# Optimization experiments

Measured on AMD Instinct MI355X. Metric: run time of the kernel, lower is better.

## Reference

```python
import jax, jax.numpy as jnp
import numpy as np
from jax import lax

T = 262144
H = 64
OUT = 16  # 2**MEMORY_LENGTH with MEMORY_LENGTH=4


def setup_inputs() -> dict:
    key = jax.random.key(0)
    ks = jax.random.split(key, 11)
    s = 0.1  # keep gates out of saturation
    return {
        "y": jax.random.normal(ks[0], (T, 1), jnp.float32),
        "W_ih0": s * jax.random.normal(ks[1], (4 * H, 1), jnp.float32),
        "W_hh0": s * jax.random.normal(ks[2], (4 * H, H), jnp.float32),
        "b_ih0": s * jax.random.normal(ks[3], (4 * H,), jnp.float32),
        "b_hh0": s * jax.random.normal(ks[4], (4 * H,), jnp.float32),
        "W_ih1": s * jax.random.normal(ks[5], (4 * H, H), jnp.float32),
        "W_hh1": s * jax.random.normal(ks[6], (4 * H, H), jnp.float32),
        "b_ih1": s * jax.random.normal(ks[7], (4 * H,), jnp.float32),
        "b_hh1": s * jax.random.normal(ks[8], (4 * H,), jnp.float32),
        "W_lin": s * jax.random.normal(ks[9], (OUT, H), jnp.float32),
        "b_lin": s * jax.random.normal(ks[10], (OUT,), jnp.float32),
    }


def _lstm_layer(x, W_ih, W_hh, b_ih, b_hh):
    # x: [T, in]. PyTorch gate order: i, f, g, o. Zero initial state.
    h = W_hh.shape[1]
    xp = x @ W_ih.T + (b_ih + b_hh)  # precompute input contribution: [T, 4H]

    def step(carry, xt):
        h_t, c_t = carry
        gates = xt + h_t @ W_hh.T
        i, f, g, o = jnp.split(gates, 4)
        i = jax.nn.sigmoid(i)
        f = jax.nn.sigmoid(f)
        g = jnp.tanh(g)
        o = jax.nn.sigmoid(o)
        c_new = f * c_t + i * g
        h_new = o * jnp.tanh(c_new)
        return (h_new, c_new), h_new

    init = (jnp.zeros((h,), x.dtype), jnp.zeros((h,), x.dtype))
    _, hs = lax.scan(step, init, xp)
    return hs  # [T, H]


def reference(y, W_ih0, W_hh0, b_ih0, b_hh0, W_ih1, W_hh1, b_ih1, b_hh1, W_lin, b_lin):
    # phase == 'train' branch of RNNDetector.forward
    h1 = _lstm_layer(y, W_ih0, W_hh0, b_ih0, b_hh0)   # [T, 64]
    h2 = _lstm_layer(h1, W_ih1, W_hh1, b_ih1, b_hh1)  # [T, 64]
    return h2 @ W_lin.T + b_lin                        # [T, 16]
```

## Files before the change

kernel.cpp:

```cpp
#include <hip/hip_runtime.h>


constexpr int T  = 262144;
constexpr int B  = 32;
constexpr int NB = T / B;
constexpr int RS = 2 * B;
constexpr int K_SS = NB + 3;

typedef _Float16 h2v  __attribute__((ext_vector_type(2)));
typedef _Float16 f16x8 __attribute__((ext_vector_type(8)));
typedef unsigned u4   __attribute__((ext_vector_type(4)));
typedef float    f4   __attribute__((ext_vector_type(4)));

__device__ __forceinline__ float rcp_f(float x) { return __builtin_amdgcn_rcpf(x); }

#define BARRIER() asm volatile("s_waitcnt lgkmcnt(0)\n\ts_barrier" ::: "memory")

static __device__ __forceinline__ float fd(unsigned w, unsigned h, float acc) {
#if __has_builtin(__builtin_amdgcn_fdot2)
  return __builtin_amdgcn_fdot2(__builtin_bit_cast(h2v, w),
                                __builtin_bit_cast(h2v, h), acc, false);
#else
  h2v a = __builtin_bit_cast(h2v, w), b = __builtin_bit_cast(h2v, h);
  acc = fmaf((float)a.x, (float)b.x, acc);
  acc = fmaf((float)a.y, (float)b.y, acc);
  return acc;
#endif
}
#define DP4(acc, W, H) { acc = fd((W).x, (H).x, acc); acc = fd((W).y, (H).y, acc); \
                         acc = fd((W).z, (H).z, acc); acc = fd((W).w, (H).w, acc); }

__device__ __forceinline__ f4 mf(u4 a, u4 b, f4 c) {
  return __builtin_amdgcn_mfma_f32_16x16x32_f16(
      __builtin_bit_cast(f16x8, a), __builtin_bit_cast(f16x8, b), c, 0, 0, 0);
}

__device__ __forceinline__ float sel4(float x0, float x1, float x2, float x3,
                                      bool b0, bool b1) {
  float lo = b0 ? x1 : x0;
  float hi = b0 ? x3 : x2;
  return b1 ? hi : lo;
}

#define DPPX1(x) __builtin_bit_cast(float, __builtin_amdgcn_mov_dpp(            \
                    __builtin_bit_cast(int, (x)), 0xB1, 0xF, 0xF, true))
#define DPPX2(x) __builtin_bit_cast(float, __builtin_amdgcn_mov_dpp(            \
                    __builtin_bit_cast(int, (x)), 0x4E, 0xF, 0xF, true))

__device__ __forceinline__ float exp2_f(float x) {
  float r; asm("v_exp_f32 %0, %1" : "=v"(r) : "v"(x)); return r;
}
__device__ __forceinline__ float exp2n_g(float u) {
  return exp2_f(fminf(-u, 126.f));
}
__device__ __forceinline__ float sig_u(float u)  { return rcp_f(1.f + exp2n_g(u)); }
__device__ __forceinline__ float tanh_u(float u) {
  float e2 = exp2n_g(u);
  return (1.f - e2) * rcp_f(1.f + e2);
}
__device__ __forceinline__ float tanh_c(float c) {
  return tanh_u(c * 2.8853900817779268f);
}

constexpr float L2E  = 1.4426950408889634f;
constexpr float L2E2 = 2.8853900817779268f;

__device__ unsigned f16rne(float f) {
  unsigned u = __float_as_uint(f);
  unsigned s = (u >> 16) & 0x8000u;
  int e = (int)((u >> 23) & 0xff) - 127;
  unsigned m = u & 0x7fffffu;
  if (e < -14) return s;
  unsigned h = s | (unsigned)((e + 15) << 10) | (m >> 13);
  unsigned rem = m & 0x1fffu;
  h += (rem > 0x1000u) || (rem == 0x1000u && (h & 1u));
  return h;
}

__global__ void pack_w(const float* __restrict__ Whh0,
                       const float* __restrict__ Whh1,
                       const float* __restrict__ Wih1,
                       const float* __restrict__ Wlin,
                       unsigned* __restrict__ ws) {
  int i = blockIdx.x * 256 + threadIdx.x;
  if (i >= 25088) return;
  float v0, v1, sc = 1.f;
  if (i < 24576) {
    int w = i >> 13, rem = i & 8191, l = rem >> 7, d = rem & 127;
    int n = d >> 3, s = (d >> 2) & 1, q = d & 3;
    int c = l & 15, g = l >> 4;
    int row = n * 16 + c;
    int col = s * 32 + 8 * g + 2 * q;
    const float* src = (w == 0) ? Whh0 : (w == 1) ? Whh1 : Wih1;
    v0 = src[row * 64 + col]; v1 = src[row * 64 + col + 1];
    sc = ((n >> 2) == 2) ? L2E2 : L2E;
  } else {
    int j = i - 24576, l = j >> 3, d = j & 7;
    int m = l >> 2, kq = l & 3, k = kq * 16 + 2 * d;
    v0 = Wlin[m * 64 + k]; v1 = Wlin[m * 64 + k + 1];
  }
  ws[i] = f16rne(v0 * sc) | (f16rne(v1 * sc) << 16);
}

#define DECLW32(wp)                                                            \
  u4 W0=(wp)[0],  W1=(wp)[1],  W2=(wp)[2],  W3=(wp)[3],                        \
     W4=(wp)[4],  W5=(wp)[5],  W6=(wp)[6],  W7=(wp)[7],                        \
     W8=(wp)[8],  W9=(wp)[9],  W10=(wp)[10],W11=(wp)[11],                      \
     W12=(wp)[12],W13=(wp)[13],W14=(wp)[14],W15=(wp)[15],                      \
     W16=(wp)[16],W17=(wp)[17],W18=(wp)[18],W19=(wp)[19],                      \
     W20=(wp)[20],W21=(wp)[21],W22=(wp)[22],W23=(wp)[23],                      \
     W24=(wp)[24],W25=(wp)[25],W26=(wp)[26],W27=(wp)[27],                      \
     W28=(wp)[28],W29=(wp)[29],W30=(wp)[30],W31=(wp)[31]

#define PINW8(a,b,c,d,e,f,g,h)                                                 \
  asm volatile("" : "+v"(a), "+v"(b), "+v"(c), "+v"(d),                        \
                    "+v"(e), "+v"(f), "+v"(g), "+v"(h))
#define PINALL() { PINW8(W0,W1,W2,W3,W4,W5,W6,W7);                             \
                   PINW8(W8,W9,W10,W11,W12,W13,W14,W15);                       \
                   PINW8(W16,W17,W18,W19,W20,W21,W22,W23);                     \
                   PINW8(W24,W25,W26,W27,W28,W29,W30,W31); }

#define MFMA16(A0u, A1u)                                                       \
  f4 a0  = mf(A0u, W0,  Z4); a0  = mf(A1u, W1,  a0);                           \
  f4 a1  = mf(A0u, W2,  Z4); a1  = mf(A1u, W3,  a1);                           \
  f4 a2  = mf(A0u, W4,  Z4); a2  = mf(A1u, W5,  a2);                           \
  f4 a3  = mf(A0u, W6,  Z4); a3  = mf(A1u, W7,  a3);                           \
  f4 a4  = mf(A0u, W8,  Z4); a4  = mf(A1u, W9,  a4);                           \
  f4 a5  = mf(A0u, W10, Z4); a5  = mf(A1u, W11, a5);                           \
  f4 a6  = mf(A0u, W12, Z4); a6  = mf(A1u, W13, a6);                           \
  f4 a7  = mf(A0u, W14, Z4); a7  = mf(A1u, W15, a7);                           \
  f4 a8  = mf(A0u, W16, Z4); a8  = mf(A1u, W17, a8);                           \
  f4 a9  = mf(A0u, W18, Z4); a9  = mf(A1u, W19, a9);                           \
  f4 a10 = mf(A0u, W20, Z4); a10 = mf(A1u, W21, a10);                          \
  f4 a11 = mf(A0u, W22, Z4); a11 = mf(A1u, W23, a11);                          \
  f4 a12 = mf(A0u, W24, Z4); a12 = mf(A1u, W25, a12);                          \
  f4 a13 = mf(A0u, W26, Z4); a13 = mf(A1u, W27, a13);                          \
  f4 a14 = mf(A0u, W28, Z4); a14 = mf(A1u, W29, a14);                          \
  f4 a15 = mf(A0u, W30, Z4); a15 = mf(A1u, W31, a15);

__global__ __launch_bounds__(256)
__attribute__((amdgpu_waves_per_eu(1, 1)))
void rnn_fused(
    const float* __restrict__ y,
    const float* __restrict__ Wih0, const float* __restrict__ bih0,
    const float* __restrict__ bhh0,
    const float* __restrict__ bih1, const float* __restrict__ bhh1,
    const float* __restrict__ blin,
    const unsigned* __restrict__ ws,
    float* __restrict__ out)
{
  const int tid = threadIdx.x;
  const int w = tid >> 6;
  __shared__ __align__(16) unsigned h0r[RS * 32];
  __shared__ __align__(16) unsigned h1r[RS * 32];
  __shared__ __align__(16) float    xpf[RS * 320];

  for (int j = tid; j < RS * 32; j += 256) { h0r[j] = 0u; h1r[j] = 0u; }
  __syncthreads();

  const f4 Z4 = {0.f, 0.f, 0.f, 0.f};

  if (w == 0) {
    __builtin_amdgcn_s_setprio(1);
    const int e = tid, g = e >> 4;
    const bool b0 = (g & 1) != 0, b1 = (g & 2) != 0;
    const u4* wp = (const u4*)(ws + e * 128);
    DECLW32(wp);
    float bbi = (bih0[e] + bhh0[e]) * L2E;
    float bbf = (bih0[64 + e] + bhh0[64 + e]) * L2E;
    float bbg = (bih0[128 + e] + bhh0[128 + e]) * L2E2;
    float bbo = (bih0[192 + e] + bhh0[192 + e]) * L2E;
    float wii = Wih0[e] * L2E, wif = Wih0[64 + e] * L2E;
    float wig = Wih0[128 + e] * L2E2, wio = Wih0[192 + e] * L2E;
    float c0 = 0.f;
    float ylv = y[e & (B - 1)];
    _Float16* h0h = (_Float16*)h0r;

    for (int k = 0; k < K_SS; ++k) {
      if (k < NB) {
        float yln = (k + 1 < NB) ? y[(k + 1) * B + (e & (B - 1))] : 0.f;
        const int base = k * B;
        #pragma unroll 1
        for (int i = 0; i < B; ++i) {
          const int s = base + i;
          PINALL();
          float ys = __builtin_bit_cast(float,
              __builtin_amdgcn_readlane(__builtin_bit_cast(int, ylv), i));
          const u4* ap = (const u4*)(h0r + ((s - 1) & (RS - 1)) * 32);
          u4 A0u = ap[g], A1u = ap[4 + g];
          MFMA16(A0u, A1u)
          float ti = sel4(a0[0],  a1[0],  a2[0],  a3[0],  b0, b1);
          float tf = sel4(a4[0],  a5[0],  a6[0],  a7[0],  b0, b1);
          float tg = sel4(a8[0],  a9[0],  a10[0], a11[0], b0, b1);
          float to = sel4(a12[0], a13[0], a14[0], a15[0], b0, b1);
          float I = sig_u(ti + fmaf(ys, wii, bbi));
          float F = sig_u(tf + fmaf(ys, wif, bbf));
          float G = tanh_u(tg + fmaf(ys, wig, bbg));
          float O = sig_u(to + fmaf(ys, wio, bbo));
          c0 = fmaf(F, c0, I * G);
          float h = O * tanh_c(c0);
          h0h[(s & (RS - 1)) * 64 + e] = (_Float16)h;
        }
        ylv = yln;
      }
      BARRIER();
    }
  } else if (w == 1 || w == 3) {
    const int e = tid & 63, g = e >> 4, c = e & 15;
    const bool b0 = (g & 1) != 0, b1 = (g & 2) != 0;
    const int ilo = (w == 1) ? 0 : 16;
    const u4* wp = (const u4*)(ws + 16384 + e * 128);
    DECLW32(wp);
    const u4* hwp = (const u4*)(ws + 24576 + e * 8);
    u4 HW0 = hwp[0], HW1 = hwp[1];
    float bbx, bby, bbz, bbw;
    {
      int R0 = (4 * g + 0) * 16 + c, R1 = (4 * g + 1) * 16 + c;
      int R2 = (4 * g + 2) * 16 + c, R3 = (4 * g + 3) * 16 + c;
      float s0 = (((4 * g + 0) >> 2) == 2) ? L2E2 : L2E;
      float s1 = (((4 * g + 1) >> 2) == 2) ? L2E2 : L2E;
      float s2 = (((4 * g + 2) >> 2) == 2) ? L2E2 : L2E;
      float s3 = (((4 * g + 3) >> 2) == 2) ? L2E2 : L2E;
      bbx = (bih1[R0] + bhh1[R0]) * s0; bby = (bih1[R1] + bhh1[R1]) * s1;
      bbz = (bih1[R2] + bhh1[R2]) * s2; bbw = (bih1[R3] + bhh1[R3]) * s3;
    }
    const int m = e >> 2, kq = e & 3;
    float bl = (kq == 0) ? blin[m] : 0.f;

    for (int k = 0; k < K_SS; ++k) {
      if (k >= 1 && k <= NB) {
        const int base = (k - 1) * B;
        #pragma unroll 1
        for (int i = ilo; i < ilo + 16; ++i) {
          const int t = base + i;
          const int slot = t & (RS - 1);
          PINALL();
          const u4* ap = (const u4*)(h0r + slot * 32);
          u4 A0u = ap[g], A1u = ap[4 + g];
          MFMA16(A0u, A1u)
          float vx = sel4(a0[0], a4[0], a8[0],  a12[0], b0, b1) + bbx;
          float vy = sel4(a1[0], a5[0], a9[0],  a13[0], b0, b1) + bby;
          float vz = sel4(a2[0], a6[0], a10[0], a14[0], b0, b1) + bbz;
          float vw = sel4(a3[0], a7[0], a11[0], a15[0], b0, b1) + bbw;
          f4 v = {vx, vy, vz, vw};
          *(f4*)(xpf + slot * 320 + c * 20 + 4 * g) = v;
        }
      }
      if (w == 3 && k >= 3) {
        const int base = (k - 3) * B;
        #pragma unroll 1
        for (int i = 0; i < B; ++i) {
          const int t = base + i;
          const int slot = t & (RS - 1);
          const u4* h1p = (const u4*)(h1r + slot * 32 + kq * 8);
          u4 X0 = h1p[0], X1 = h1p[1];
          float r2 = 0.f;
          DP4(r2, HW0, X0) DP4(r2, HW1, X1)
          r2 += DPPX1(r2);
          r2 += DPPX2(r2);
          if (kq == 0) out[t * 16 + m] = r2 + bl;
        }
      }
      BARRIER();
    }
  } else {
    __builtin_amdgcn_s_setprio(1);
    const int e = tid - 128, g = e >> 4, c = e & 15;
    const bool b0 = (g & 1) != 0, b1 = (g & 2) != 0;
    const u4* wp = (const u4*)(ws + 8192 + e * 128);
    DECLW32(wp);
    float c1 = 0.f;
    _Float16* h1h = (_Float16*)h1r;

    for (int k = 0; k < K_SS; ++k) {
      if (k >= 2 && k <= NB + 1) {
        const int base = (k - 2) * B;
        #pragma unroll 1
        for (int i = 0; i < B; ++i) {
          const int t = base + i;
          const int slot = t & (RS - 1);
          PINALL();
          const float* xb = xpf + slot * 320 + c * 20;
          float xi = xb[g], xf = xb[4 + g], xg2 = xb[8 + g], xo = xb[12 + g];
          const u4* ap = (const u4*)(h1r + ((t - 1) & (RS - 1)) * 32);
          u4 A0u = ap[g], A1u = ap[4 + g];
          MFMA16(A0u, A1u)
          float ti = sel4(a0[0],  a1[0],  a2[0],  a3[0],  b0, b1);
          float tf = sel4(a4[0],  a5[0],  a6[0],  a7[0],  b0, b1);
          float tg = sel4(a8[0],  a9[0],  a10[0], a11[0], b0, b1);
          float to = sel4(a12[0], a13[0], a14[0], a15[0], b0, b1);
          float I = sig_u(ti + xi);
          float F = sig_u(tf + xf);
          float G = tanh_u(tg + xg2);
          float O = sig_u(to + xo);
          c1 = fmaf(F, c1, I * G);
          float h = O * tanh_c(c1);
          h1h[slot * 64 + e] = (_Float16)h;
        }
      }
      BARRIER();
    }
  }
}

extern "C" void kernel_launch(void* const* d_in, const int* in_sizes, int n_in,
                              void* d_out, int out_size, void* d_ws, size_t ws_size,
                              hipStream_t stream) {
  const float* y    = (const float*)d_in[0];
  const float* Wih0 = (const float*)d_in[1];
  const float* Whh0 = (const float*)d_in[2];
  const float* bih0 = (const float*)d_in[3];
  const float* bhh0 = (const float*)d_in[4];
  const float* Wih1 = (const float*)d_in[5];
  const float* Whh1 = (const float*)d_in[6];
  const float* bih1 = (const float*)d_in[7];
  const float* bhh1 = (const float*)d_in[8];
  const float* Wlin = (const float*)d_in[9];
  const float* blin = (const float*)d_in[10];
  unsigned* ws = (unsigned*)d_ws;

  pack_w<<<dim3(98), dim3(256), 0, stream>>>(Whh0, Whh1, Wih1, Wlin, ws);
  rnn_fused<<<dim3(1), dim3(256), 0, stream>>>(
      y, Wih0, bih0, bhh0, bih1, bhh1, blin, ws, (float*)d_out);
}
```

Baseline: 109.2 ms.

## Fuse layer-0 and layer-1 recurrences into one wave with interleaved steps

New measurement: 208.4 ms. 90.9% more time.

```diff
diff --git a/kernel.cpp b/kernel.cpp
--- a/kernel.cpp
+++ b/kernel.cpp
@@ -11,6 +11,9 @@
 typedef _Float16 f16x8 __attribute__((ext_vector_type(8)));
 typedef unsigned u4   __attribute__((ext_vector_type(4)));
 typedef float    f4   __attribute__((ext_vector_type(4)));
+
+struct TT { static constexpr bool value = true; };
+struct FF { static constexpr bool value = false; };
 
 __device__ __forceinline__ float rcp_f(float x) { return __builtin_amdgcn_rcpf(x); }
 
@@ -112,13 +115,30 @@
      W24=(wp)[24],W25=(wp)[25],W26=(wp)[26],W27=(wp)[27],                      \
      W28=(wp)[28],W29=(wp)[29],W30=(wp)[30],W31=(wp)[31]
 
+#define DECLX32(wp)                                                            \
+  u4 X0=(wp)[0],  X1=(wp)[1],  X2=(wp)[2],  X3=(wp)[3],                        \
+     X4=(wp)[4],  X5=(wp)[5],  X6=(wp)[6],  X7=(wp)[7],                        \
+     X8=(wp)[8],  X9=(wp)[9],  X10=(wp)[10],X11=(wp)[11],                      \
+     X12=(wp)[12],X13=(wp)[13],X14=(wp)[14],X15=(wp)[15],                      \
+     X16=(wp)[16],X17=(wp)[17],X18=(wp)[18],X19=(wp)[19],                      \
+     X20=(wp)[20],X21=(wp)[21],X22=(wp)[22],X23=(wp)[23],                      \
+     X24=(wp)[24],X25=(wp)[25],X26=(wp)[26],X27=(wp)[27],                      \
+     X28=(wp)[28],X29=(wp)[29],X30=(wp)[30],X31=(wp)[31]
+
 #define PINW8(a,b,c,d,e,f,g,h)                                                 \
   asm volatile("" : "+v"(a), "+v"(b), "+v"(c), "+v"(d),                        \
                     "+v"(e), "+v"(f), "+v"(g), "+v"(h))
-#define PINALL() { PINW8(W0,W1,W2,W3,W4,W5,W6,W7);                             \
-                   PINW8(W8,W9,W10,W11,W12,W13,W14,W15);                       \
-                   PINW8(W16,W17,W18,W19,W20,W21,W22,W23);                     \
-                   PINW8(W24,W25,W26,W27,W28,W29,W30,W31); }
+#define PINA8(a,b,c,d,e,f,g,h)                                                 \
+  asm volatile("" : "+a"(a), "+a"(b), "+a"(c), "+a"(d),                        \
+                    "+a"(e), "+a"(f), "+a"(g), "+a"(h))
+#define PINALLW() { PINW8(W0,W1,W2,W3,W4,W5,W6,W7);                            \
+                    PINW8(W8,W9,W10,W11,W12,W13,W14,W15);                      \
+                    PINW8(W16,W17,W18,W19,W20,W21,W22,W23);                    \
+                    PINW8(W24,W25,W26,W27,W28,W29,W30,W31); }
+#define PINALLX() { PINA8(X0,X1,X2,X3,X4,X5,X6,X7);                            \
+                    PINA8(X8,X9,X10,X11,X12,X13,X14,X15);                      \
+                    PINA8(X16,X17,X18,X19,X20,X21,X22,X23);                    \
+                    PINA8(X24,X25,X26,X27,X28,X29,X30,X31); }
 
 #define MFMA16(A0u, A1u)                                                       \
   f4 a0  = mf(A0u, W0,  Z4); a0  = mf(A1u, W1,  a0);                           \
@@ -138,6 +158,24 @@
   f4 a14 = mf(A0u, W28, Z4); a14 = mf(A1u, W29, a14);                          \
   f4 a15 = mf(A0u, W30, Z4); a15 = mf(A1u, W31, a15);
 
+#define MFMA16X(A0u, A1u)                                                      \
+  f4 xa0  = mf(A0u, X0,  Z4); xa0  = mf(A1u, X1,  xa0);                        \
+  f4 xa1  = mf(A0u, X2,  Z4); xa1  = mf(A1u, X3,  xa1);                        \
+  f4 xa2  = mf(A0u, X4,  Z4); xa2  = mf(A1u, X5,  xa2);                        \
+  f4 xa3  = mf(A0u, X6,  Z4); xa3  = mf(A1u, X7,  xa3);                        \
+  f4 xa4  = mf(A0u, X8,  Z4); xa4  = mf(A1u, X9,  xa4);                        \
+  f4 xa5  = mf(A0u, X10, Z4); xa5  = mf(A1u, X11, xa5);                        \
+  f4 xa6  = mf(A0u, X12, Z4); xa6  = mf(A1u, X13, xa6);                        \
+  f4 xa7  = mf(A0u, X14, Z4); xa7  = mf(A1u, X15, xa7);                        \
+  f4 xa8  = mf(A0u, X16, Z4); xa8  = mf(A1u, X17, xa8);                        \
+  f4 xa9  = mf(A0u, X18, Z4); xa9  = mf(A1u, X19, xa9);                        \
+  f4 xa10 = mf(A0u, X20, Z4); xa10 = mf(A1u, X21, xa10);                       \
+  f4 xa11 = mf(A0u, X22, Z4); xa11 = mf(A1u, X23, xa11);                       \
+  f4 xa12 = mf(A0u, X24, Z4); xa12 = mf(A1u, X25, xa12);                       \
+  f4 xa13 = mf(A0u, X26, Z4); xa13 = mf(A1u, X27, xa13);                       \
+  f4 xa14 = mf(A0u, X28, Z4); xa14 = mf(A1u, X29, xa14);                       \
+  f4 xa15 = mf(A0u, X30, Z4); xa15 = mf(A1u, X31, xa15);
+
 __global__ __launch_bounds__(256)
 __attribute__((amdgpu_waves_per_eu(1, 1)))
 void rnn_fused(
@@ -162,28 +200,31 @@
 
   if (w == 0) {
     __builtin_amdgcn_s_setprio(1);
-    const int e = tid, g = e >> 4;
+    const int e = tid, g = e >> 4, c = e & 15;
     const bool b0 = (g & 1) != 0, b1 = (g & 2) != 0;
-    const u4* wp = (const u4*)(ws + e * 128);
-    DECLW32(wp);
+    const u4* wpA = (const u4*)(ws + e * 128);
+    const u4* wpB = (const u4*)(ws + 8192 + e * 128);
+    DECLW32(wpA);
+    DECLX32(wpB);
     float bbi = (bih0[e] + bhh0[e]) * L2E;
     float bbf = (bih0[64 + e] + bhh0[64 + e]) * L2E;
     float bbg = (bih0[128 + e] + bhh0[128 + e]) * L2E2;
     float bbo = (bih0[192 + e] + bhh0[192 + e]) * L2E;
     float wii = Wih0[e] * L2E, wif = Wih0[64 + e] * L2E;
     float wig = Wih0[128 + e] * L2E2, wio = Wih0[192 + e] * L2E;
-    float c0 = 0.f;
+    float c0 = 0.f, c1 = 0.f;
     float ylv = y[e & (B - 1)];
     _Float16* h0h = (_Float16*)h0r;
-
-    for (int k = 0; k < K_SS; ++k) {
-      if (k < NB) {
-        float yln = (k + 1 < NB) ? y[(k + 1) * B + (e & (B - 1))] : 0.f;
-        const int base = k * B;
-        #pragma unroll 1
-        for (int i = 0; i < B; ++i) {
-          const int s = base + i;
-          PINALL();
+    _Float16* h1h = (_Float16*)h1r;
+
+    auto blk = [&](auto L0C, auto L1C, int k) {
+      constexpr bool DL0 = decltype(L0C)::value;
+      constexpr bool DL1 = decltype(L1C)::value;
+      #pragma unroll 1
+      for (int i = 0; i < B; ++i) {
+        PINALLW(); PINALLX();
+        if constexpr (DL0) {
+          const int s = k * B + i;
           float ys = __builtin_bit_cast(float,
               __builtin_amdgcn_readlane(__builtin_bit_cast(int, ylv), i));
           const u4* ap = (const u4*)(h0r + ((s - 1) & (RS - 1)) * 32);
@@ -201,8 +242,37 @@
           float h = O * tanh_c(c0);
           h0h[(s & (RS - 1)) * 64 + e] = (_Float16)h;
         }
-        ylv = yln;
+        if constexpr (DL1) {
+          const int t = k * B + i - 2 * B;
+          const int slot = t & (RS - 1);
+          const float* xb = xpf + slot * 320 + c * 20;
+          float xi = xb[g], xf = xb[4 + g], xg2 = xb[8 + g], xo = xb[12 + g];
+          const u4* jp = (const u4*)(h1r + ((t - 1) & (RS - 1)) * 32);
+          u4 J0u = jp[g], J1u = jp[4 + g];
+          MFMA16X(J0u, J1u)
+          float ti = sel4(xa0[0],  xa1[0],  xa2[0],  xa3[0],  b0, b1);
+          float tf = sel4(xa4[0],  xa5[0],  xa6[0],  xa7[0],  b0, b1);
+          float tg = sel4(xa8[0],  xa9[0],  xa10[0], xa11[0], b0, b1);
+          float to = sel4(xa12[0], xa13[0], xa14[0], xa15[0], b0, b1);
+          float I = sig_u(ti + xi);
+          float F = sig_u(tf + xf);
+          float G = tanh_u(tg + xg2);
+          float O = sig_u(to + xo);
+          c1 = fmaf(F, c1, I * G);
+          float h = O * tanh_c(c1);
+          h1h[slot * 64 + e] = (_Float16)h;
+        }
       }
+    };
+
+    for (int k = 0; k < K_SS; ++k) {
+      const bool l0 = (k < NB);
+      const bool l1 = (k >= 2 && k <= NB + 1);
+      float yln = (l0 && k + 1 < NB) ? y[(k + 1) * B + (e & (B - 1))] : 0.f;
+      if (l0 && l1)      blk(TT{}, TT{}, k);
+      else if (l0)       blk(TT{}, FF{}, k);
+      else if (l1)       blk(FF{}, TT{}, k);
+      ylv = yln;
       BARRIER();
     }
   } else if (w == 1 || w == 3) {
@@ -211,8 +281,6 @@
     const int ilo = (w == 1) ? 0 : 16;
     const u4* wp = (const u4*)(ws + 16384 + e * 128);
     DECLW32(wp);
-    const u4* hwp = (const u4*)(ws + 24576 + e * 8);
-    u4 HW0 = hwp[0], HW1 = hwp[1];
     float bbx, bby, bbz, bbw;
     {
       int R0 = (4 * g + 0) * 16 + c, R1 = (4 * g + 1) * 16 + c;
@@ -224,8 +292,6 @@
       bbx = (bih1[R0] + bhh1[R0]) * s0; bby = (bih1[R1] + bhh1[R1]) * s1;
       bbz = (bih1[R2] + bhh1[R2]) * s2; bbw = (bih1[R3] + bhh1[R3]) * s3;
     }
-    const int m = e >> 2, kq = e & 3;
-    float bl = (kq == 0) ? blin[m] : 0.f;
 
     for (int k = 0; k < K_SS; ++k) {
       if (k >= 1 && k <= NB) {
@@ -234,7 +300,7 @@
         for (int i = ilo; i < ilo + 16; ++i) {
           const int t = base + i;
           const int slot = t & (RS - 1);
-          PINALL();
+          PINALLW();
           const u4* ap = (const u4*)(h0r + slot * 32);
           u4 A0u = ap[g], A1u = ap[4 + g];
           MFMA16(A0u, A1u)
@@ -246,56 +312,29 @@
           *(f4*)(xpf + slot * 320 + c * 20 + 4 * g) = v;
         }
       }
-      if (w == 3 && k >= 3) {
+      BARRIER();
+    }
+  } else {
+    const int e = tid & 63;
+    const u4* hwp = (const u4*)(ws + 24576 + e * 8);
+    u4 HW0 = hwp[0], HW1 = hwp[1];
+    const int m = e >> 2, kq = e & 3;
+    float bl = (kq == 0) ? blin[m] : 0.f;
+
+    for (int k = 0; k < K_SS; ++k) {
+      if (k >= 3) {
         const int base = (k - 3) * B;
         #pragma unroll 1
         for (int i = 0; i < B; ++i) {
           const int t = base + i;
           const int slot = t & (RS - 1);
           const u4* h1p = (const u4*)(h1r + slot * 32 + kq * 8);
-          u4 X0 = h1p[0], X1 = h1p[1];
+          u4 Y0 = h1p[0], Y1 = h1p[1];
           float r2 = 0.f;
-          DP4(r2, HW0, X0) DP4(r2, HW1, X1)
+          DP4(r2, HW0, Y0) DP4(r2, HW1, Y1)
           r2 += DPPX1(r2);
           r2 += DPPX2(r2);
           if (kq == 0) out[t * 16 + m] = r2 + bl;
-        }
-      }
-      BARRIER();
-    }
-  } else {
-    __builtin_amdgcn_s_setprio(1);
-    const int e = tid - 128, g = e >> 4, c = e & 15;
-    const bool b0 = (g & 1) != 0, b1 = (g & 2) != 0;
-    const u4* wp = (const u4*)(ws + 8192 + e * 128);
-    DECLW32(wp);
-    float c1 = 0.f;
-    _Float16* h1h = (_Float16*)h1r;
-
-    for (int k = 0; k < K_SS; ++k) {
-      if (k >= 2 && k <= NB + 1) {
-        const int base = (k - 2) * B;
-        #pragma unroll 1
-        for (int i = 0; i < B; ++i) {
-          const int t = base + i;
-          const int slot = t & (RS - 1);
-          PINALL();
-          const float* xb = xpf + slot * 320 + c * 20;
-          float xi = xb[g], xf = xb[4 + g], xg2 = xb[8 + g], xo = xb[12 + g];
-          const u4* ap = (const u4*)(h1r + ((t - 1) & (RS - 1)) * 32);
-          u4 A0u = ap[g], A1u = ap[4 + g];
-          MFMA16(A0u, A1u)
-          float ti = sel4(a0[0],  a1[0],  a2[0],  a3[0],  b0, b1);
-          float tf = sel4(a4[0],  a5[0],  a6[0],  a7[0],  b0, b1);
-          float tg = sel4(a8[0],  a9[0],  a10[0], a11[0], b0, b1);
-          float to = sel4(a12[0], a13[0], a14[0], a15[0], b0, b1);
-          float I = sig_u(ti + xi);
-          float F = sig_u(tf + xf);
-          float G = tanh_u(tg + xg2);
-          float O = sig_u(to + xo);
-          c1 = fmaf(F, c1, I * G);
-          float h = O * tanh_c(c1);
-          h1h[slot * 64 + e] = (_Float16)h;
         }
       }
       BARRIER();
```
